# Kernel tuning notes

Measured on AMD Instinct MI355X. Metric: run time of the kernel, lower is better.

Reference implementation:

```python
import jax, jax.numpy as jnp
import numpy as np

W_MAE, W_GRAD, W_TV, W_BG, W_MSE = 1.0, 0.1, 0.002, 0.15, 1.0
EPS = 1e-8


def setup_inputs() -> dict:
    key = jax.random.key(0)
    k1, k2, k3 = jax.random.split(key, 3)
    B, C, D, H, W = 2, 3, 128, 128, 128
    pred = jax.random.normal(k1, (B, C, D, H, W), dtype=jnp.float32)
    target = jax.random.normal(k2, (B, C, D, H, W), dtype=jnp.float32)
    # binary foreground mask, broadcast over channels
    mask = (jax.random.uniform(k3, (B, 1, D, H, W)) > 0.5).astype(jnp.float32)
    return {"pred": pred, "target": target, "mask": mask}


def _grad3(x):
    dx = x[:, :, 1:, :, :] - x[:, :, :-1, :, :]
    dy = x[:, :, :, 1:, :] - x[:, :, :, :-1, :]
    dz = x[:, :, :, :, 1:] - x[:, :, :, :, :-1]
    return dx, dy, dz


def reference(pred, target, mask):
    C = pred.shape[1]

    def masked_mean(x, m):
        return (x * m).sum() / (m.sum() * C + EPS)

    pred_in = pred * mask
    tgt_in = target * mask
    diff = pred_in - tgt_in

    l_mae = masked_mean(jnp.abs(diff), mask)

    px, py, pz = _grad3(pred_in)
    tx, ty, tz = _grad3(tgt_in)
    mx = jnp.minimum(mask[:, :, 1:, :, :], mask[:, :, :-1, :, :])
    my = jnp.minimum(mask[:, :, :, 1:, :], mask[:, :, :, :-1, :])
    mz = jnp.minimum(mask[:, :, :, :, 1:], mask[:, :, :, :, :-1])

    l_grad = (masked_mean(jnp.abs(px - tx), mx)
              + masked_mean(jnp.abs(py - ty), my)
              + masked_mean(jnp.abs(pz - tz), mz))
    l_tv = (masked_mean(jnp.abs(px), mx)
            + masked_mean(jnp.abs(py), my)
            + masked_mean(jnp.abs(pz), mz))

    inv = 1.0 - mask
    l_bg = (jnp.abs(pred) * inv).sum() / (inv.sum() * C + EPS)

    l_mse = masked_mean(diff ** 2, mask)

    return (W_MAE * l_mae + W_GRAD * l_grad + W_TV * l_tv
            + W_BG * l_bg + W_MSE * l_mse)
```

## Files before the change

### kernel.cpp

```cpp
#include <hip/hip_runtime.h>

#define NACC 13
#define NPAD 16
#define NBLOCKS 4096
#define NMID 16

__device__ __forceinline__ float4 ld4(const float* p) {
    return *reinterpret_cast<const float4*>(p);
}

__global__ __launch_bounds__(256) void loss_main(
    const float* __restrict__ pred, const float* __restrict__ target,
    const float* __restrict__ mask, float* __restrict__ partials)
{
    float acc[NACC];
#pragma unroll
    for (int k = 0; k < NACC; ++k) acc[k] = 0.f;

    const float4 z4 = make_float4(0.f, 0.f, 0.f, 0.f);

    const int xcd     = blockIdx.x & 7;
    const int local   = blockIdx.x >> 3;
    const int d       = (xcd << 4) + (local >> 5);
    const int q       = ((local & 31) << 8) + threadIdx.x;
    const int w4      = q & 31;
    const int h       = (q >> 5) & 127;
    const int b       = q >> 12;
    const int w       = w4 << 2;
    const int mb  = b * 2097152 + d * 16384 + h * 128 + w;
    const int pb0 = b * 6291456 + d * 16384 + h * 128 + w;
    const bool hw = w4 < 31, hh = h < 127, hd = d < 127;

    const float4 m0  = ld4(mask + mb);
    const float  m4w = hw ? mask[mb + 4] : 0.f;
    const float4 mh  = hh ? ld4(mask + mb + 128)   : z4;
    const float4 md  = hd ? ld4(mask + mb + 16384) : z4;

    const float mz0 = fminf(m0.x, m0.y), mz1 = fminf(m0.y, m0.z),
                mz2 = fminf(m0.z, m0.w), mz3 = fminf(m0.w, m4w);
    const float my0 = fminf(m0.x, mh.x), my1 = fminf(m0.y, mh.y),
                my2 = fminf(m0.z, mh.z), my3 = fminf(m0.w, mh.w);
    const float mx0 = fminf(m0.x, md.x), mx1 = fminf(m0.y, md.y),
                mx2 = fminf(m0.z, md.z), mx3 = fminf(m0.w, md.w);

    acc[0] = m0.x + m0.y + m0.z + m0.w;
    acc[1] = mx0 + mx1 + mx2 + mx3;
    acc[2] = my0 + my1 + my2 + my3;
    acc[3] = mz0 + mz1 + mz2 + mz3;

#pragma unroll
    for (int c = 0; c < 3; ++c) {
        const int pb = pb0 + c * 2097152;
        const float4 p0 = ld4(pred + pb);
        const float4 t0 = ld4(target + pb);
        float p4 = 0.f, t4 = 0.f;
        if (hw) { p4 = pred[pb + 4]; t4 = target[pb + 4]; }
        const float4 ph = hh ? ld4(pred + pb + 128)     : z4;
        const float4 th = hh ? ld4(target + pb + 128)   : z4;
        const float4 pd = hd ? ld4(pred + pb + 16384)   : z4;
        const float4 td = hd ? ld4(target + pb + 16384) : z4;

        const float e0x = p0.x - t0.x, e0y = p0.y - t0.y,
                    e0z = p0.z - t0.z, e0w = p0.w - t0.w;
        const float e4  = p4 - t4;

        acc[4] += fabsf(e0x)*m0.x + fabsf(e0y)*m0.y
                + fabsf(e0z)*m0.z + fabsf(e0w)*m0.w;
        acc[5] += e0x*e0x*m0.x + e0y*e0y*m0.y
                + e0z*e0z*m0.z + e0w*e0w*m0.w;
        acc[6] += fabsf(p0.x)*(1.f-m0.x) + fabsf(p0.y)*(1.f-m0.y)
                + fabsf(p0.z)*(1.f-m0.z) + fabsf(p0.w)*(1.f-m0.w);

        acc[9]  += fabsf(e0y-e0x)*mz0 + fabsf(e0z-e0y)*mz1
                 + fabsf(e0w-e0z)*mz2 + fabsf(e4 -e0w)*mz3;
        acc[12] += fabsf(p0.y-p0.x)*mz0 + fabsf(p0.z-p0.y)*mz1
                 + fabsf(p0.w-p0.z)*mz2 + fabsf(p4  -p0.w)*mz3;

        acc[8]  += fabsf((ph.x-th.x)-e0x)*my0 + fabsf((ph.y-th.y)-e0y)*my1
                 + fabsf((ph.z-th.z)-e0z)*my2 + fabsf((ph.w-th.w)-e0w)*my3;
        acc[11] += fabsf(ph.x-p0.x)*my0 + fabsf(ph.y-p0.y)*my1
                 + fabsf(ph.z-p0.z)*my2 + fabsf(ph.w-p0.w)*my3;

        acc[7]  += fabsf((pd.x-td.x)-e0x)*mx0 + fabsf((pd.y-td.y)-e0y)*mx1
                 + fabsf((pd.z-td.z)-e0z)*mx2 + fabsf((pd.w-td.w)-e0w)*mx3;
        acc[10] += fabsf(pd.x-p0.x)*mx0 + fabsf(pd.y-p0.y)*mx1
                 + fabsf(pd.z-p0.z)*mx2 + fabsf(pd.w-p0.w)*mx3;
    }

    const int lane = threadIdx.x & 63;
    const int wave = threadIdx.x >> 6;
    __shared__ float red[4][NACC];
#pragma unroll
    for (int k = 0; k < NACC; ++k) {
        float v = acc[k];
        for (int o = 32; o > 0; o >>= 1) v += __shfl_down(v, o, 64);
        if (lane == 0) red[wave][k] = v;
    }
    __syncthreads();
    if (threadIdx.x < NPAD) {
        const int k = threadIdx.x;
        const float v = (k < NACC)
            ? red[0][k] + red[1][k] + red[2][k] + red[3][k] : 0.f;
        partials[blockIdx.x * NPAD + k] = v;
    }
}

__global__ __launch_bounds__(256) void loss_mid(
    const float* __restrict__ partials, float* __restrict__ mid)
{
    const int r = blockIdx.x * 256 + threadIdx.x;
    const float* row = partials + r * NPAD;
    const float4 r0 = ld4(row);     const float4 r1 = ld4(row + 4);
    const float4 r2 = ld4(row + 8); const float4 r3 = ld4(row + 12);
    float acc[NPAD] = {r0.x, r0.y, r0.z, r0.w, r1.x, r1.y, r1.z, r1.w,
                       r2.x, r2.y, r2.z, r2.w, r3.x, r3.y, r3.z, r3.w};

    const int lane = threadIdx.x & 63;
    const int wave = threadIdx.x >> 6;
    __shared__ float red[4][NPAD];
#pragma unroll
    for (int k = 0; k < NPAD; ++k) {
        float v = acc[k];
        for (int o = 32; o > 0; o >>= 1) v += __shfl_down(v, o, 64);
        if (lane == 0) red[wave][k] = v;
    }
    __syncthreads();
    if (threadIdx.x < NPAD) {
        const int k = threadIdx.x;
        mid[blockIdx.x * NPAD + k] =
            red[0][k] + red[1][k] + red[2][k] + red[3][k];
    }
}

__global__ __launch_bounds__(64) void loss_final(
    const float* __restrict__ mid, float* __restrict__ out)
{
    const int lane = threadIdx.x;
    float acc[NPAD];
#pragma unroll
    for (int k = 0; k < NPAD; ++k) acc[k] = 0.f;
    if (lane < NMID) {
        const float* row = mid + lane * NPAD;
        const float4 r0 = ld4(row);     const float4 r1 = ld4(row + 4);
        const float4 r2 = ld4(row + 8); const float4 r3 = ld4(row + 12);
        acc[0] = r0.x;  acc[1] = r0.y;  acc[2] = r0.z;  acc[3] = r0.w;
        acc[4] = r1.x;  acc[5] = r1.y;  acc[6] = r1.z;  acc[7] = r1.w;
        acc[8] = r2.x;  acc[9] = r2.y;  acc[10] = r2.z; acc[11] = r2.w;
        acc[12] = r3.x; acc[13] = r3.y; acc[14] = r3.z; acc[15] = r3.w;
    }
#pragma unroll
    for (int k = 0; k < NACC; ++k) {
        for (int o = 32; o > 0; o >>= 1) acc[k] += __shfl_down(acc[k], o, 64);
    }
    if (lane == 0) {
        const float EPS = 1e-8f;
        const float M = acc[0], Mx = acc[1], My = acc[2], Mz = acc[3];
        float loss = (acc[4] + acc[5]) / (3.f * M + EPS);
        loss += 0.1f   * (acc[7] / (3.f*Mx + EPS) + acc[8] / (3.f*My + EPS)
                        + acc[9] / (3.f*Mz + EPS));
        loss += 0.002f * (acc[10] / (3.f*Mx + EPS) + acc[11] / (3.f*My + EPS)
                        + acc[12] / (3.f*Mz + EPS));
        const float inv = 4194304.f - M;
        loss += 0.15f * acc[6] / (3.f * inv + EPS);
        out[0] = loss;
    }
}

extern "C" void kernel_launch(void* const* d_in, const int* in_sizes, int n_in,
                              void* d_out, int out_size, void* d_ws, size_t ws_size,
                              hipStream_t stream) {
    const float* pred   = (const float*)d_in[0];
    const float* target = (const float*)d_in[1];
    const float* mask   = (const float*)d_in[2];
    float* out      = (float*)d_out;
    float* partials = (float*)d_ws;
    float* mid      = partials + NBLOCKS * NPAD;

    loss_main<<<NBLOCKS, 256, 0, stream>>>(pred, target, mask, partials);
    loss_mid<<<NMID, 256, 0, stream>>>(partials, mid);
    loss_final<<<1, 64, 0, stream>>>(mid, out);
}
```

Measured before the change: 150.9 us.

## Make neighbor loads branchless via clamped offsets and linear block indexing

Replaces the conditional boundary loads with unconditional loads whose offset collapses to zero at the edge. The boundary masks are multiplied by 0/1 validity factors instead, which removes divergent branches and exec-mask handling around the global loads. It also drops the XCD-aware block-to-depth-slice swizzle in favor of plain linear indexing. That likely changes L2 locality for the depth-neighbor reads across chiplets.

```diff
diff --git a/kernel.cpp b/kernel.cpp
--- a/kernel.cpp
+++ b/kernel.cpp
@@ -17,31 +17,33 @@
 #pragma unroll
     for (int k = 0; k < NACC; ++k) acc[k] = 0.f;
 
-    const float4 z4 = make_float4(0.f, 0.f, 0.f, 0.f);
-
-    const int xcd     = blockIdx.x & 7;
-    const int local   = blockIdx.x >> 3;
-    const int d       = (xcd << 4) + (local >> 5);
-    const int q       = ((local & 31) << 8) + threadIdx.x;
-    const int w4      = q & 31;
-    const int h       = (q >> 5) & 127;
-    const int b       = q >> 12;
-    const int w       = w4 << 2;
+    const int g  = blockIdx.x * 256 + threadIdx.x;
+    const int w4 = g & 31;
+    const int h  = (g >> 5) & 127;
+    const int d  = (g >> 12) & 127;
+    const int b  = g >> 19;
+    const int w  = w4 << 2;
     const int mb  = b * 2097152 + d * 16384 + h * 128 + w;
     const int pb0 = b * 6291456 + d * 16384 + h * 128 + w;
-    const bool hw = w4 < 31, hh = h < 127, hd = d < 127;
+
+    const float wv = (w4 < 31) ? 1.f : 0.f;
+    const float hv = (h < 127) ? 1.f : 0.f;
+    const float dv = (d < 127) ? 1.f : 0.f;
+    const int ow = (w4 < 31) ? 4     : 0;
+    const int oh = (h < 127) ? 128   : 0;
+    const int od = (d < 127) ? 16384 : 0;
 
     const float4 m0  = ld4(mask + mb);
-    const float  m4w = hw ? mask[mb + 4] : 0.f;
-    const float4 mh  = hh ? ld4(mask + mb + 128)   : z4;
-    const float4 md  = hd ? ld4(mask + mb + 16384) : z4;
+    const float4 mh  = ld4(mask + mb + oh);
+    const float4 md  = ld4(mask + mb + od);
+    const float  m4w = mask[mb + ow];
 
     const float mz0 = fminf(m0.x, m0.y), mz1 = fminf(m0.y, m0.z),
-                mz2 = fminf(m0.z, m0.w), mz3 = fminf(m0.w, m4w);
-    const float my0 = fminf(m0.x, mh.x), my1 = fminf(m0.y, mh.y),
-                my2 = fminf(m0.z, mh.z), my3 = fminf(m0.w, mh.w);
-    const float mx0 = fminf(m0.x, md.x), mx1 = fminf(m0.y, md.y),
-                mx2 = fminf(m0.z, md.z), mx3 = fminf(m0.w, md.w);
+                mz2 = fminf(m0.z, m0.w), mz3 = fminf(m0.w, m4w) * wv;
+    const float my0 = fminf(m0.x, mh.x) * hv, my1 = fminf(m0.y, mh.y) * hv,
+                my2 = fminf(m0.z, mh.z) * hv, my3 = fminf(m0.w, mh.w) * hv;
+    const float mx0 = fminf(m0.x, md.x) * dv, mx1 = fminf(m0.y, md.y) * dv,
+                mx2 = fminf(m0.z, md.z) * dv, mx3 = fminf(m0.w, md.w) * dv;
 
     acc[0] = m0.x + m0.y + m0.z + m0.w;
     acc[1] = mx0 + mx1 + mx2 + mx3;
@@ -53,12 +55,12 @@
         const int pb = pb0 + c * 2097152;
         const float4 p0 = ld4(pred + pb);
         const float4 t0 = ld4(target + pb);
-        float p4 = 0.f, t4 = 0.f;
-        if (hw) { p4 = pred[pb + 4]; t4 = target[pb + 4]; }
-        const float4 ph = hh ? ld4(pred + pb + 128)     : z4;
-        const float4 th = hh ? ld4(target + pb + 128)   : z4;
-        const float4 pd = hd ? ld4(pred + pb + 16384)   : z4;
-        const float4 td = hd ? ld4(target + pb + 16384) : z4;
+        const float  p4 = pred[pb + ow];
+        const float  t4 = target[pb + ow];
+        const float4 ph = ld4(pred + pb + oh);
+        const float4 th = ld4(target + pb + oh);
+        const float4 pd = ld4(pred + pb + od);
+        const float4 td = ld4(target + pb + od);
 
         const float e0x = p0.x - t0.x, e0y = p0.y - t0.y,
                     e0z = p0.z - t0.z, e0w = p0.w - t0.w;
```

Result: faster. 147.9 us (-2.0%).
